# Kernel tuning notes

Measured on AMD Instinct MI355X. Metric: run time of the kernel, lower is better.

## Reference

```python
import jax, jax.numpy as jnp
import numpy as np

E, H, I, T = 8, 2048, 1408, 16384  # experts, hidden, intermediate, total tokens


def setup_inputs() -> dict:
    key = jax.random.key(0)
    kx, kg, kd = jax.random.split(key, 3)
    x = jax.random.normal(kx, (T, H), dtype=jnp.float32)
    # trunc_normal(std=0.02) approximated by scaled normal params
    gate_up_proj = jax.random.normal(kg, (E, 2 * I, H), dtype=jnp.float32) * 0.02
    down_proj = jax.random.normal(kd, (E, H, I), dtype=jnp.float32) * 0.02
    num_tokens_per_expert = jnp.full((E,), T // E, dtype=jnp.int32)
    return {
        "x": x,
        "gate_up_proj": gate_up_proj,
        "down_proj": down_proj,
        "num_tokens_per_expert": num_tokens_per_expert,
    }


def reference(x, gate_up_proj, down_proj, num_tokens_per_expert):
    # torch._grouped_mm(x, W.transpose(-2,-1), offs=cumsum(counts)) is exactly
    # a ragged grouped GEMM over contiguous per-expert token segments.
    xb = x.astype(jnp.bfloat16)
    # rhs for ragged_dot: [groups, k, n] = [E, H, 2I]
    gu_w = gate_up_proj.astype(jnp.bfloat16).transpose(0, 2, 1)
    gate_up = jax.lax.ragged_dot(xb, gu_w, num_tokens_per_expert)  # [T, 2I]
    gate, up = jnp.split(gate_up, 2, axis=-1)
    h = jax.nn.silu(gate) * up  # [T, I] bf16, fused SiLU-gate
    dn_w = down_proj.astype(jnp.bfloat16).transpose(0, 2, 1)  # [E, I, H]
    out = jax.lax.ragged_dot(h, dn_w, num_tokens_per_expert)  # [T, H]
    return out.astype(x.dtype)
```

## Files before the change

kernel.cpp:

```cpp
#include <hip/hip_runtime.h>
#include <cstdint>
#include <cstddef>

#define TT 16384
#define HH 2048
#define II 1408
#define EE 8

typedef __attribute__((ext_vector_type(4))) float f32x4;
typedef __attribute__((ext_vector_type(8))) short bf16x8;
typedef __attribute__((ext_vector_type(4))) short s16x4;
typedef __attribute__((ext_vector_type(8))) short s16x8;

__device__ __forceinline__ short f2bf(float f) {
  union { float f; unsigned u; } v; v.f = f;
  unsigned u = v.u;
  return (short)((u + 0x7fffu + ((u >> 16) & 1u)) >> 16);
}
__device__ __forceinline__ float bf2f(short s) {
  union { unsigned u; float f; } v;
  v.u = ((unsigned)(unsigned short)s) << 16;
  return v.f;
}

__device__ __forceinline__ void find_tile(const int* __restrict__ counts, int mt,
                                          int& e_out, int& row_base, int& rows_valid) {
  int off = 0, acc = 0, e = -1, rb = 0, rv = 0;
#pragma unroll
  for (int ee = 0; ee < EE; ++ee) {
    int n = counts[ee];
    int tiles = (n + 127) >> 7;
    if (e < 0 && mt < acc + tiles) {
      e = ee;
      int lmt = mt - acc;
      rb = off + (lmt << 7);
      rv = n - (lmt << 7);
      rv = rv > 128 ? 128 : rv;
    }
    acc += tiles;
    off += n;
  }
  e_out = e; row_base = rb; rows_valid = rv;
}

__global__ __launch_bounds__(256, 2)
void moe_gemm1(const float* __restrict__ x, const float* __restrict__ gup,
               const int* __restrict__ counts, short* __restrict__ h) {
  __shared__ short As[128][32];
  __shared__ short Bg[64][32];
  __shared__ short Bu[64][32];

  const int tid  = threadIdx.x;
  const int lane = tid & 63;
  const int wid  = tid >> 6;
  const int wr   = wid >> 1;
  const int wc   = wid & 1;

  int e, row_base, rows_valid;
  find_tile(counts, blockIdx.x, e, row_base, rows_valid);
  if (e < 0 || rows_valid <= 0) return;

  const int nt = blockIdx.y;
  const size_t wbase = (size_t)e * (2 * II) * HH;
  const int jg = nt * 64;
  const int ju = II + nt * 64;

  f32x4 a_st[4], bg_st[2], bu_st[2];

  auto load_tiles = [&](int kb) {
#pragma unroll
    for (int i = 0; i < 4; ++i) {
      int q = tid + 256 * i;
      int r = q >> 3, kq = q & 7;
      int gr = row_base + ((r < rows_valid) ? r : 0);
      a_st[i] = *reinterpret_cast<const f32x4*>(&x[(size_t)gr * HH + kb + kq * 4]);
    }
#pragma unroll
    for (int i = 0; i < 2; ++i) {
      int q = tid + 256 * i;
      int r = q >> 3, kq = q & 7;
      bg_st[i] = *reinterpret_cast<const f32x4*>(&gup[wbase + (size_t)(jg + r) * HH + kb + kq * 4]);
      bu_st[i] = *reinterpret_cast<const f32x4*>(&gup[wbase + (size_t)(ju + r) * HH + kb + kq * 4]);
    }
  };

  auto write_tiles = [&]() {
#pragma unroll
    for (int i = 0; i < 4; ++i) {
      int q = tid + 256 * i;
      int r = q >> 3, kq = q & 7;
      s16x4 p;
      p[0] = f2bf(a_st[i][0]); p[1] = f2bf(a_st[i][1]);
      p[2] = f2bf(a_st[i][2]); p[3] = f2bf(a_st[i][3]);
      *reinterpret_cast<s16x4*>(&As[r][kq * 4]) = p;
    }
#pragma unroll
    for (int i = 0; i < 2; ++i) {
      int q = tid + 256 * i;
      int r = q >> 3, kq = q & 7;
      s16x4 pg, pu;
      pg[0] = f2bf(bg_st[i][0]); pg[1] = f2bf(bg_st[i][1]);
      pg[2] = f2bf(bg_st[i][2]); pg[3] = f2bf(bg_st[i][3]);
      pu[0] = f2bf(bu_st[i][0]); pu[1] = f2bf(bu_st[i][1]);
      pu[2] = f2bf(bu_st[i][2]); pu[3] = f2bf(bu_st[i][3]);
      *reinterpret_cast<s16x4*>(&Bg[r][kq * 4]) = pg;
      *reinterpret_cast<s16x4*>(&Bu[r][kq * 4]) = pu;
    }
  };

  f32x4 accg[4][2], accu[4][2];
  const f32x4 z = {0.f, 0.f, 0.f, 0.f};
#pragma unroll
  for (int m = 0; m < 4; ++m)
#pragma unroll
    for (int n = 0; n < 2; ++n) { accg[m][n] = z; accu[m][n] = z; }

  const int NK = HH / 32;
  load_tiles(0);
  for (int ks = 0; ks < NK; ++ks) {
    __syncthreads();
    write_tiles();
    if (ks + 1 < NK) load_tiles((ks + 1) * 32);
    __syncthreads();

    bf16x8 a[4], bg[2], bu[2];
    const int ko = (lane >> 4) * 8;
    const int rl = lane & 15;
#pragma unroll
    for (int m = 0; m < 4; ++m)
      a[m] = *reinterpret_cast<const bf16x8*>(&As[wr * 64 + m * 16 + rl][ko]);
#pragma unroll
    for (int n = 0; n < 2; ++n) {
      bg[n] = *reinterpret_cast<const bf16x8*>(&Bg[wc * 32 + n * 16 + rl][ko]);
      bu[n] = *reinterpret_cast<const bf16x8*>(&Bu[wc * 32 + n * 16 + rl][ko]);
    }
#pragma unroll
    for (int m = 0; m < 4; ++m)
#pragma unroll
      for (int n = 0; n < 2; ++n) {
        accg[m][n] = __builtin_amdgcn_mfma_f32_16x16x32_bf16(a[m], bg[n], accg[m][n], 0, 0, 0);
        accu[m][n] = __builtin_amdgcn_mfma_f32_16x16x32_bf16(a[m], bu[n], accu[m][n], 0, 0, 0);
      }
  }

  const int rl = lane & 15;
#pragma unroll
  for (int m = 0; m < 4; ++m) {
#pragma unroll
    for (int r = 0; r < 4; ++r) {
      int lr = wr * 64 + m * 16 + (lane >> 4) * 4 + r;
      if (lr < rows_valid) {
        size_t row = (size_t)(row_base + lr);
#pragma unroll
        for (int n = 0; n < 2; ++n) {
          float gf = bf2f(f2bf(accg[m][n][r]));
          float uf = bf2f(f2bf(accu[m][n][r]));
          float hv = gf / (1.0f + expf(-gf)) * uf;
          h[row * II + jg + wc * 32 + n * 16 + rl] = f2bf(hv);
        }
      }
    }
  }
}

__global__ __launch_bounds__(256, 2)
void moe_gemm2(const short* __restrict__ h, const float* __restrict__ dp,
               const int* __restrict__ counts, float* __restrict__ out) {
  __shared__ short As[128][32];
  __shared__ short Bs[128][32];

  const int tid  = threadIdx.x;
  const int lane = tid & 63;
  const int wid  = tid >> 6;
  const int wr   = wid >> 1;
  const int wc   = wid & 1;

  int e, row_base, rows_valid;
  find_tile(counts, blockIdx.x, e, row_base, rows_valid);
  if (e < 0 || rows_valid <= 0) return;

  const int nb = blockIdx.y * 128;
  const size_t wbase = (size_t)e * HH * II;

  s16x8 a_st[2];
  f32x4 b_st[4];

  auto load_tiles = [&](int kb) {
#pragma unroll
    for (int i = 0; i < 2; ++i) {
      int q = tid + 256 * i;
      int r = q >> 2, kh = q & 3;
      int gr = row_base + ((r < rows_valid) ? r : 0);
      a_st[i] = *reinterpret_cast<const s16x8*>(&h[(size_t)gr * II + kb + kh * 8]);
    }
#pragma unroll
    for (int i = 0; i < 4; ++i) {
      int q = tid + 256 * i;
      int r = q >> 3, kq = q & 7;
      b_st[i] = *reinterpret_cast<const f32x4*>(&dp[wbase + (size_t)(nb + r) * II + kb + kq * 4]);
    }
  };

  auto write_tiles = [&]() {
#pragma unroll
    for (int i = 0; i < 2; ++i) {
      int q = tid + 256 * i;
      int r = q >> 2, kh = q & 3;
      *reinterpret_cast<s16x8*>(&As[r][kh * 8]) = a_st[i];
    }
#pragma unroll
    for (int i = 0; i < 4; ++i) {
      int q = tid + 256 * i;
      int r = q >> 3, kq = q & 7;
      s16x4 p;
      p[0] = f2bf(b_st[i][0]); p[1] = f2bf(b_st[i][1]);
      p[2] = f2bf(b_st[i][2]); p[3] = f2bf(b_st[i][3]);
      *reinterpret_cast<s16x4*>(&Bs[r][kq * 4]) = p;
    }
  };

  f32x4 acc[4][4];
  const f32x4 z = {0.f, 0.f, 0.f, 0.f};
#pragma unroll
  for (int m = 0; m < 4; ++m)
#pragma unroll
    for (int n = 0; n < 4; ++n) acc[m][n] = z;

  const int NK = II / 32;
  load_tiles(0);
  for (int ks = 0; ks < NK; ++ks) {
    __syncthreads();
    write_tiles();
    if (ks + 1 < NK) load_tiles((ks + 1) * 32);
    __syncthreads();

    bf16x8 a[4], b[4];
    const int ko = (lane >> 4) * 8;
    const int rl = lane & 15;
#pragma unroll
    for (int m = 0; m < 4; ++m)
      a[m] = *reinterpret_cast<const bf16x8*>(&As[wr * 64 + m * 16 + rl][ko]);
#pragma unroll
    for (int n = 0; n < 4; ++n)
      b[n] = *reinterpret_cast<const bf16x8*>(&Bs[wc * 64 + n * 16 + rl][ko]);
#pragma unroll
    for (int m = 0; m < 4; ++m)
#pragma unroll
      for (int n = 0; n < 4; ++n)
        acc[m][n] = __builtin_amdgcn_mfma_f32_16x16x32_bf16(a[m], b[n], acc[m][n], 0, 0, 0);
  }

  const int rl = lane & 15;
#pragma unroll
  for (int m = 0; m < 4; ++m) {
#pragma unroll
    for (int r = 0; r < 4; ++r) {
      int lr = wr * 64 + m * 16 + (lane >> 4) * 4 + r;
      if (lr < rows_valid) {
        size_t row = (size_t)(row_base + lr);
#pragma unroll
        for (int n = 0; n < 4; ++n) {
          out[row * HH + nb + wc * 64 + n * 16 + rl] = bf2f(f2bf(acc[m][n][r]));
        }
      }
    }
  }
}

extern "C" void kernel_launch(void* const* d_in, const int* in_sizes, int n_in,
                              void* d_out, int out_size, void* d_ws, size_t ws_size,
                              hipStream_t stream) {
  const float* x      = (const float*)d_in[0];
  const float* gup    = (const float*)d_in[1];
  const float* dp     = (const float*)d_in[2];
  const int*   counts = (const int*)d_in[3];
  float* out = (float*)d_out;
  short* h   = (short*)d_ws;

  const int MT_MAX = (TT + 127) / 128 + EE;

  moe_gemm1<<<dim3(MT_MAX, II / 64), dim3(256), 0, stream>>>(x, gup, counts, h);
  moe_gemm2<<<dim3(MT_MAX, HH / 128), dim3(256), 0, stream>>>(h, dp, counts, out);
}
```

Measured before the change: 1.035 ms.

## Double-buffer LDS, swizzle shared layout, remap blocks for XCD locality, packed bf16 convert

Both GEMM kernels now double-buffer their shared-memory tiles, so each k-step needs one barrier instead of two and the next tile is written while the current one is consumed. The LDS layout is XOR-swizzled to avoid bank conflicts on the 16-byte MFMA operand reads. The grid is flattened and remapped so consecutive blocks on the same XCD share A/B tiles. The software bf16 rounding is replaced with the packed v_cvt_pk_bf16_f32 instruction. In exchange, LDS use doubles and the min-occupancy hint of 2 is dropped, which may reduce occupancy.

```diff
diff --git a/kernel.cpp b/kernel.cpp
--- a/kernel.cpp
+++ b/kernel.cpp
@@ -21,6 +21,17 @@
   union { unsigned u; float f; } v;
   v.u = ((unsigned)(unsigned short)s) << 16;
   return v.f;
+}
+__device__ __forceinline__ unsigned pk_bf16(float lo, float hi) {
+  unsigned r;
+  asm("v_cvt_pk_bf16_f32 %0, %1, %2" : "=v"(r) : "v"(lo), "v"(hi));
+  return r;
+}
+__device__ __forceinline__ void cvt4(void* dst, const f32x4 v) {
+  union { s16x4 s; unsigned u[2]; } p;
+  p.u[0] = pk_bf16(v[0], v[1]);
+  p.u[1] = pk_bf16(v[2], v[3]);
+  *reinterpret_cast<s16x4*>(dst) = p.s;
 }
 
 __device__ __forceinline__ void find_tile(const int* __restrict__ counts, int mt,
@@ -43,12 +54,16 @@
   e_out = e; row_base = rb; rows_valid = rv;
 }
 
-__global__ __launch_bounds__(256, 2)
+__device__ __forceinline__ int swz_off(int r, int kq) {
+  return r * 64 + ((((kq >> 1) ^ (r & 3))) << 4) + ((kq & 1) << 3);
+}
+
+__global__ __launch_bounds__(256)
 void moe_gemm1(const float* __restrict__ x, const float* __restrict__ gup,
                const int* __restrict__ counts, short* __restrict__ h) {
-  __shared__ short As[128][32];
-  __shared__ short Bg[64][32];
-  __shared__ short Bu[64][32];
+  __shared__ short As[2][128 * 32];
+  __shared__ short Bg[2][64 * 32];
+  __shared__ short Bu[2][64 * 32];
 
   const int tid  = threadIdx.x;
   const int lane = tid & 63;
@@ -56,11 +71,16 @@
   const int wr   = wid >> 1;
   const int wc   = wid & 1;
 
+  const int NT = II / 64;
+  const int NB = ((TT + 127) / 128 + EE) * NT;
+  const int l  = ((int)blockIdx.x % 8) * (NB / 8) + (int)blockIdx.x / 8;
+  const int nt = l % NT;
+  const int mt = l / NT;
+
   int e, row_base, rows_valid;
-  find_tile(counts, blockIdx.x, e, row_base, rows_valid);
+  find_tile(counts, mt, e, row_base, rows_valid);
   if (e < 0 || rows_valid <= 0) return;
 
-  const int nt = blockIdx.y;
   const size_t wbase = (size_t)e * (2 * II) * HH;
   const int jg = nt * 64;
   const int ju = II + nt * 64;
@@ -84,27 +104,20 @@
     }
   };
 
-  auto write_tiles = [&]() {
+  auto write_tiles = [&](int b) {
 #pragma unroll
     for (int i = 0; i < 4; ++i) {
       int q = tid + 256 * i;
       int r = q >> 3, kq = q & 7;
-      s16x4 p;
-      p[0] = f2bf(a_st[i][0]); p[1] = f2bf(a_st[i][1]);
-      p[2] = f2bf(a_st[i][2]); p[3] = f2bf(a_st[i][3]);
-      *reinterpret_cast<s16x4*>(&As[r][kq * 4]) = p;
+      cvt4((char*)As[b] + swz_off(r, kq), a_st[i]);
     }
 #pragma unroll
     for (int i = 0; i < 2; ++i) {
       int q = tid + 256 * i;
       int r = q >> 3, kq = q & 7;
-      s16x4 pg, pu;
-      pg[0] = f2bf(bg_st[i][0]); pg[1] = f2bf(bg_st[i][1]);
-      pg[2] = f2bf(bg_st[i][2]); pg[3] = f2bf(bg_st[i][3]);
-      pu[0] = f2bf(bu_st[i][0]); pu[1] = f2bf(bu_st[i][1]);
-      pu[2] = f2bf(bu_st[i][2]); pu[3] = f2bf(bu_st[i][3]);
-      *reinterpret_cast<s16x4*>(&Bg[r][kq * 4]) = pg;
-      *reinterpret_cast<s16x4*>(&Bu[r][kq * 4]) = pu;
+      int off = swz_off(r, kq);
+      cvt4((char*)Bg[b] + off, bg_st[i]);
+      cvt4((char*)Bu[b] + off, bu_st[i]);
     }
   };
 
@@ -115,24 +128,26 @@
 #pragma unroll
     for (int n = 0; n < 2; ++n) { accg[m][n] = z; accu[m][n] = z; }
 
+  const int g  = lane >> 4;
+  const int rl = lane & 15;
+  const int su = ((g ^ (rl & 3)) << 4);
+
   const int NK = HH / 32;
   load_tiles(0);
+  write_tiles(0);
+  load_tiles(32);
+  __syncthreads();
+
+  int cur = 0;
   for (int ks = 0; ks < NK; ++ks) {
-    __syncthreads();
-    write_tiles();
-    if (ks + 1 < NK) load_tiles((ks + 1) * 32);
-    __syncthreads();
-
     bf16x8 a[4], bg[2], bu[2];
-    const int ko = (lane >> 4) * 8;
-    const int rl = lane & 15;
 #pragma unroll
     for (int m = 0; m < 4; ++m)
-      a[m] = *reinterpret_cast<const bf16x8*>(&As[wr * 64 + m * 16 + rl][ko]);
+      a[m] = *reinterpret_cast<const bf16x8*>((const char*)As[cur] + (wr * 64 + m * 16 + rl) * 64 + su);
 #pragma unroll
     for (int n = 0; n < 2; ++n) {
-      bg[n] = *reinterpret_cast<const bf16x8*>(&Bg[wc * 32 + n * 16 + rl][ko]);
-      bu[n] = *reinterpret_cast<const bf16x8*>(&Bu[wc * 32 + n * 16 + rl][ko]);
+      bg[n] = *reinterpret_cast<const bf16x8*>((const char*)Bg[cur] + (wc * 32 + n * 16 + rl) * 64 + su);
+      bu[n] = *reinterpret_cast<const bf16x8*>((const char*)Bu[cur] + (wc * 32 + n * 16 + rl) * 64 + su);
     }
 #pragma unroll
     for (int m = 0; m < 4; ++m)
@@ -141,9 +156,14 @@
         accg[m][n] = __builtin_amdgcn_mfma_f32_16x16x32_bf16(a[m], bg[n], accg[m][n], 0, 0, 0);
         accu[m][n] = __builtin_amdgcn_mfma_f32_16x16x32_bf16(a[m], bu[n], accu[m][n], 0, 0, 0);
       }
-  }
-
-  const int rl = lane & 15;
+    if (ks + 1 < NK) {
+      write_tiles(cur ^ 1);
+      if (ks + 2 < NK) load_tiles((ks + 2) * 32);
+    }
+    __syncthreads();
+    cur ^= 1;
+  }
+
 #pragma unroll
   for (int m = 0; m < 4; ++m) {
 #pragma unroll
@@ -163,11 +183,11 @@
   }
 }
 
-__global__ __launch_bounds__(256, 2)
+__global__ __launch_bounds__(256)
 void moe_gemm2(const short* __restrict__ h, const float* __restrict__ dp,
                const int* __restrict__ counts, float* __restrict__ out) {
-  __shared__ short As[128][32];
-  __shared__ short Bs[128][32];
+  __shared__ short As[2][128 * 32];
+  __shared__ short Bs[2][128 * 32];
 
   const int tid  = threadIdx.x;
   const int lane = tid & 63;
@@ -175,11 +195,17 @@
   const int wr   = wid >> 1;
   const int wc   = wid & 1;
 
+  const int NT = HH / 128;
+  const int NB = ((TT + 127) / 128 + EE) * NT;
+  const int l  = ((int)blockIdx.x % 8) * (NB / 8) + (int)blockIdx.x / 8;
+  const int nt = l % NT;
+  const int mt = l / NT;
+
   int e, row_base, rows_valid;
-  find_tile(counts, blockIdx.x, e, row_base, rows_valid);
+  find_tile(counts, mt, e, row_base, rows_valid);
   if (e < 0 || rows_valid <= 0) return;
 
-  const int nb = blockIdx.y * 128;
+  const int nb = nt * 128;
   const size_t wbase = (size_t)e * HH * II;
 
   s16x8 a_st[2];
@@ -201,21 +227,18 @@
     }
   };
 
-  auto write_tiles = [&]() {
+  auto write_tiles = [&](int b) {
 #pragma unroll
     for (int i = 0; i < 2; ++i) {
       int q = tid + 256 * i;
       int r = q >> 2, kh = q & 3;
-      *reinterpret_cast<s16x8*>(&As[r][kh * 8]) = a_st[i];
+      *reinterpret_cast<s16x8*>((char*)As[b] + r * 64 + ((kh ^ (r & 3)) << 4)) = a_st[i];
     }
 #pragma unroll
     for (int i = 0; i < 4; ++i) {
       int q = tid + 256 * i;
       int r = q >> 3, kq = q & 7;
-      s16x4 p;
-      p[0] = f2bf(b_st[i][0]); p[1] = f2bf(b_st[i][1]);
-      p[2] = f2bf(b_st[i][2]); p[3] = f2bf(b_st[i][3]);
-      *reinterpret_cast<s16x4*>(&Bs[r][kq * 4]) = p;
+      cvt4((char*)Bs[b] + swz_off(r, kq), b_st[i]);
     }
   };
 
@@ -226,31 +249,38 @@
 #pragma unroll
     for (int n = 0; n < 4; ++n) acc[m][n] = z;
 
+  const int g  = lane >> 4;
+  const int rl = lane & 15;
+  const int su = ((g ^ (rl & 3)) << 4);
+
   const int NK = II / 32;
   load_tiles(0);
+  write_tiles(0);
+  load_tiles(32);
+  __syncthreads();
+
+  int cur = 0;
   for (int ks = 0; ks < NK; ++ks) {
-    __syncthreads();
-    write_tiles();
-    if (ks + 1 < NK) load_tiles((ks + 1) * 32);
-    __syncthreads();
-
     bf16x8 a[4], b[4];
-    const int ko = (lane >> 4) * 8;
-    const int rl = lane & 15;
 #pragma unroll
     for (int m = 0; m < 4; ++m)
-      a[m] = *reinterpret_cast<const bf16x8*>(&As[wr * 64 + m * 16 + rl][ko]);
+      a[m] = *reinterpret_cast<const bf16x8*>((const char*)As[cur] + (wr * 64 + m * 16 + rl) * 64 + su);
 #pragma unroll
     for (int n = 0; n < 4; ++n)
-      b[n] = *reinterpret_cast<const bf16x8*>(&Bs[wc * 64 + n * 16 + rl][ko]);
+      b[n] = *reinterpret_cast<const bf16x8*>((const char*)Bs[cur] + (wc * 64 + n * 16 + rl) * 64 + su);
 #pragma unroll
     for (int m = 0; m < 4; ++m)
 #pragma unroll
       for (int n = 0; n < 4; ++n)
         acc[m][n] = __builtin_amdgcn_mfma_f32_16x16x32_bf16(a[m], b[n], acc[m][n], 0, 0, 0);
-  }
-
-  const int rl = lane & 15;
+    if (ks + 1 < NK) {
+      write_tiles(cur ^ 1);
+      if (ks + 2 < NK) load_tiles((ks + 2) * 32);
+    }
+    __syncthreads();
+    cur ^= 1;
+  }
+
 #pragma unroll
   for (int m = 0; m < 4; ++m) {
 #pragma unroll
@@ -278,7 +308,9 @@
   short* h   = (short*)d_ws;
 
   const int MT_MAX = (TT + 127) / 128 + EE;
-
-  moe_gemm1<<<dim3(MT_MAX, II / 64), dim3(256), 0, stream>>>(x, gup, counts, h);
-  moe_gemm2<<<dim3(MT_MAX, HH / 128), dim3(256), 0, stream>>>(h, dp, counts, out);
-}
+  const int NB1 = MT_MAX * (II / 64);
+  const int NB2 = MT_MAX * (HH / 128);
+
+  moe_gemm1<<<dim3(NB1), dim3(256), 0, stream>>>(x, gup, counts, h);
+  moe_gemm2<<<dim3(NB2), dim3(256), 0, stream>>>(h, dp, counts, out);
+}
```

After: 920.5 us. 1.12x faster.
